# Performance work log

Measured on AMD Instinct MI355X. Metric: run time of the kernel, lower is better.

## Reference

```python
import jax, jax.numpy as jnp
import numpy as np

N_HEAD, D_MODEL, D_K, D_V = 8, 512, 64, 64
B, S = 4, 2048
LN_EPS = 1e-5


def setup_inputs() -> dict:
    key = jax.random.key(0)
    ks = jax.random.split(key, 12)
    std_qk = np.sqrt(2.0 / (D_MODEL + D_K))
    std_v = np.sqrt(2.0 / (D_MODEL + D_V))
    return {
        "q": jax.random.normal(ks[0], (B, S, D_MODEL), jnp.float32),
        "k": jax.random.normal(ks[1], (B, S, D_MODEL), jnp.float32),
        "v": jax.random.normal(ks[2], (B, S, D_MODEL), jnp.float32),
        "w_qs": jax.random.normal(ks[3], (N_HEAD * D_K, D_MODEL), jnp.float32) * std_qk,
        "b_qs": jnp.zeros((N_HEAD * D_K,), jnp.float32),
        "w_ks": jax.random.normal(ks[4], (N_HEAD * D_K, D_MODEL), jnp.float32) * std_qk,
        "b_ks": jnp.zeros((N_HEAD * D_K,), jnp.float32),
        "w_vs": jax.random.normal(ks[5], (N_HEAD * D_V, D_MODEL), jnp.float32) * std_v,
        "b_vs": jnp.zeros((N_HEAD * D_V,), jnp.float32),
        "w_fc": jax.random.normal(ks[6], (D_MODEL, N_HEAD * D_V), jnp.float32) * np.sqrt(2.0 / (D_MODEL + N_HEAD * D_V)),
        "b_fc": jnp.zeros((D_MODEL,), jnp.float32),
        "ln_g": jnp.ones((D_MODEL,), jnp.float32),
        "ln_b": jnp.zeros((D_MODEL,), jnp.float32),
    }


def reference(q, k, v, w_qs, b_qs, w_ks, b_ks, w_vs, b_vs, w_fc, b_fc, ln_g, ln_b):
    sz_b, len_q, _ = q.shape
    residual = q
    temperature = np.power(D_K, 0.5).astype(np.float32)
    # Projections: [b, s, h*dk] -> [h, b, s, dk]  (matches permute(2,0,1,3))
    qh = (jnp.einsum('bsd,fd->bsf', q, w_qs) + b_qs).reshape(sz_b, len_q, N_HEAD, D_K).transpose(2, 0, 1, 3)
    kh = (jnp.einsum('bsd,fd->bsf', k, w_ks) + b_ks).reshape(sz_b, -1, N_HEAD, D_K).transpose(2, 0, 1, 3)
    vh = (jnp.einsum('bsd,fd->bsf', v, w_vs) + b_vs).reshape(sz_b, -1, N_HEAD, D_V).transpose(2, 0, 1, 3)
    # Scaled dot-product attention (dropout is identity in eval)
    attn = jnp.einsum('hbqd,hbkd->hbqk', qh, kh) / temperature
    attn = jax.nn.softmax(attn, axis=-1)
    out = jnp.einsum('hbqk,hbkv->hbqv', attn, vh)          # [h, b, q, dv]
    out = out.transpose(1, 2, 0, 3).reshape(sz_b, len_q, N_HEAD * D_V)
    out = jnp.einsum('bsf,df->bsd', out, w_fc) + b_fc
    # Residual + LayerNorm
    x = out + residual
    mu = jnp.mean(x, axis=-1, keepdims=True)
    var = jnp.mean(jnp.square(x - mu), axis=-1, keepdims=True)
    x = (x - mu) * jax.lax.rsqrt(var + LN_EPS) * ln_g + ln_b
    # attn returned as [(n_head*b), len_q, len_k] to match torch bmm layout
    return x, attn.reshape(N_HEAD * sz_b, len_q, -1)
```

## Files before the change

kernel.cpp:

```cpp
#include <hip/hip_runtime.h>
#include <hip/hip_bf16.h>

constexpr int NB  = 4;
constexpr int NS  = 2048;
constexpr int NH  = 8;
constexpr int DM  = 512;
constexpr int DKV = 64;
constexpr int HB  = NH * NB;

typedef __attribute__((ext_vector_type(8))) short short8;
typedef __attribute__((ext_vector_type(4))) float f32x4;

__device__ inline unsigned short f2bf(float f) {
    unsigned u = __builtin_bit_cast(unsigned, f);
    u = (u + 0x7fffu + ((u >> 16) & 1u)) >> 16;
    return (unsigned short)u;
}
__device__ inline float bf2f(unsigned short h) {
    unsigned u = ((unsigned)h) << 16;
    return __builtin_bit_cast(float, u);
}
__device__ inline short8 ld8(const unsigned short* p) { return *(const short8*)p; }

__device__ inline short8 pack8(const float* p) {
    f32x4 a = *(const f32x4*)p;
    f32x4 b = *(const f32x4*)(p + 4);
    short8 r;
    r[0] = (short)f2bf(a[0]); r[1] = (short)f2bf(a[1]);
    r[2] = (short)f2bf(a[2]); r[3] = (short)f2bf(a[3]);
    r[4] = (short)f2bf(b[0]); r[5] = (short)f2bf(b[1]);
    r[6] = (short)f2bf(b[2]); r[7] = (short)f2bf(b[3]);
    return r;
}

__device__ inline f32x4 mfma16(short8 a, short8 b, f32x4 c) {
    return __builtin_amdgcn_mfma_f32_16x16x32_bf16(a, b, c, 0, 0, 0);
}

__device__ inline void gl_lds16(const void* g, void* l) {
    __builtin_amdgcn_global_load_lds(
        (const __attribute__((address_space(1))) unsigned*)g,
        (__attribute__((address_space(3))) unsigned*)l, 16, 0, 0);
}

__device__ inline void bar() { __builtin_amdgcn_s_barrier(); }

__global__ __launch_bounds__(256) void k_cvt(const float* __restrict__ x0,
                                             const float* __restrict__ x1,
                                             const float* __restrict__ x2,
                                             const float* __restrict__ w0,
                                             const float* __restrict__ w1,
                                             const float* __restrict__ w2,
                                             const float* __restrict__ w3,
                                             unsigned short* __restrict__ dx0,
                                             unsigned short* __restrict__ dx1,
                                             unsigned short* __restrict__ dx2,
                                             unsigned short* __restrict__ dw0,
                                             unsigned short* __restrict__ dw1,
                                             unsigned short* __restrict__ dw2,
                                             unsigned short* __restrict__ dw3)
{
    const float* s; unsigned short* d; size_t i;
    if (blockIdx.y < 3) {
        switch (blockIdx.y) {
            case 0:  s = x0; d = dx0; break;
            case 1:  s = x1; d = dx1; break;
            default: s = x2; d = dx2; break;
        }
        i = ((size_t)blockIdx.x * 256 + threadIdx.x) * 8;
    } else {
        if (blockIdx.x >= 512) return;
        switch (blockIdx.x >> 7) {
            case 0:  s = w0; d = dw0; break;
            case 1:  s = w1; d = dw1; break;
            case 2:  s = w2; d = dw2; break;
            default: s = w3; d = dw3; break;
        }
        i = ((size_t)(blockIdx.x & 127) * 256 + threadIdx.x) * 8;
    }
    *(short8*)(d + i) = pack8(s + i);
}

__global__ __launch_bounds__(256, 4) void k_proj(const unsigned short* __restrict__ X,
                                              const unsigned short* __restrict__ W,
                                              const float* __restrict__ bias,
                                              unsigned short* __restrict__ out,
                                              float scale, int vtrans)
{
    const int tid = threadIdx.x;
    const int l = tid & 63, w = tid >> 6;
    const int c = l & 15, g = l >> 4;
    const int m0 = blockIdx.y * 64 + w * 16;
    const int f0 = blockIdx.x * 64;
    const int arow = m0 + c;

    f32x4 acc[4] = {};
    const unsigned short* aB = X + (size_t)arow * DM;
    for (int kb = 0; kb < DM; kb += 32) {
        short8 af = ld8(aB + kb + g * 8);
#pragma unroll
        for (int n = 0; n < 4; ++n) {
            short8 bf = ld8(W + (size_t)(f0 + n * 16 + c) * DM + kb + g * 8);
            acc[n] = mfma16(af, bf, acc[n]);
        }
    }
#pragma unroll
    for (int n = 0; n < 4; ++n) {
        const int f = f0 + n * 16 + c;
        const int h = f >> 6, d = f & 63;
        const float bv = bias[f];
#pragma unroll
        for (int r = 0; r < 4; ++r) {
            const int m = m0 + g * 4 + r;
            const int bb = m >> 11, s = m & (NS - 1);
            const int hb = h * NB + bb;
            const float v = (acc[n][r] + bv) * scale;
            const size_t idx = vtrans ? ((size_t)(hb * DKV + d) * NS + s)
                                      : ((size_t)(hb * NS + s) * DKV + d);
            out[idx] = f2bf(v);
        }
    }
}

__global__ __launch_bounds__(256, 4) void k_attn(const unsigned short* __restrict__ Qh,
                                                 const unsigned short* __restrict__ Kh,
                                                 const unsigned short* __restrict__ Vt,
                                                 float* __restrict__ attn,
                                                 unsigned short* __restrict__ Obuf)
{
    __shared__ __align__(16) char kld[2][8192];
    __shared__ __align__(16) char vld[2][8192];
    __shared__ __align__(16) char plds[4 * 2048];
    const int tid = threadIdx.x;
    const int l = tid & 63, w = tid >> 6;
    const int c = l & 15, g = l >> 4;
    constexpr int NT = NS / 64;

    const int bid = blockIdx.x;
    const int wid = (bid & 7) * 128 + (bid >> 3);
    const int hb = wid >> 5;
    const int q0 = (wid & 31) * 64 + w * 16;
    char* myp = plds + w * 2048;

    const char* kbytes = (const char*)(Kh + (size_t)hb * NS * DKV);
    const char* vbytes = (const char*)(Vt + (size_t)hb * DKV * NS);

    const unsigned short* qb = Qh + ((size_t)hb * NS + q0 + c) * DKV + g * 8;
    const short8 qf0 = ld8(qb), qf1 = ld8(qb + 32);

    int koff[2], voff[2];
#pragma unroll
    for (int j = 0; j < 2; ++j) {
        const int D = (w * 2 + j) * 1024 + l * 16;
        const int row = D >> 7;
        const int scolb = (D & 127) ^ ((row & 7) << 4);
        koff[j] = row * 128 + scolb;
        voff[j] = row * (NS * 2) + scolb;
    }
    const int swc = (c & 7) << 4;

    const int ldsbase = w * 2048;

    float ls[4] = {0.f, 0.f, 0.f, 0.f};
    {
        gl_lds16(kbytes + koff[0], kld[0] + ldsbase);
        gl_lds16(kbytes + koff[1], kld[0] + ldsbase + 1024);
        asm volatile("s_waitcnt vmcnt(0)" ::: "memory");
        bar();
        __builtin_amdgcn_sched_barrier(0);
        int cur = 0;
        for (int kt = 0; kt < NT; ++kt) {
            if (kt + 1 < NT) {
                const size_t nb = (size_t)(kt + 1) * 64 * 128;
                gl_lds16(kbytes + nb + koff[0], kld[cur ^ 1] + ldsbase);
                gl_lds16(kbytes + nb + koff[1], kld[cur ^ 1] + ldsbase + 1024);
            }
            if (kt > 0) {
                if (kt + 1 < NT) { asm volatile("s_waitcnt vmcnt(2)" ::: "memory"); }
                else             { asm volatile("s_waitcnt vmcnt(0)" ::: "memory"); }
                bar();
                __builtin_amdgcn_sched_barrier(0);
            }
#pragma unroll
            for (int t = 0; t < 4; ++t) {
                const int rb = (t * 16 + c) * 128;
                const short8 b0 = *(const short8*)(kld[cur] + rb + ((g * 16) ^ swc));
                const short8 b1 = *(const short8*)(kld[cur] + rb + ((64 + g * 16) ^ swc));
                f32x4 z = {};
                z = mfma16(qf0, b0, z);
                z = mfma16(qf1, b1, z);
#pragma unroll
                for (int r = 0; r < 4; ++r) ls[r] += exp2f(z[r]);
            }
            bar();
            cur ^= 1;
        }
    }
    float li[4];
#pragma unroll
    for (int r = 0; r < 4; ++r) {
        float s = ls[r];
        s += __shfl_xor(s, 1);
        s += __shfl_xor(s, 2);
        s += __shfl_xor(s, 4);
        s += __shfl_xor(s, 8);
        li[r] = 1.0f / s;
    }

    f32x4 oacc[4] = {};
    const int srow = l >> 2, sseg = l & 3;
    float* srowp = attn + (size_t)hb * NS * NS + (size_t)(q0 + srow) * NS + sseg * 16;
    const int swsr = (srow & 7) << 4;

    {
        gl_lds16(kbytes + koff[0], kld[0] + ldsbase);
        gl_lds16(kbytes + koff[1], kld[0] + ldsbase + 1024);
        gl_lds16(vbytes + voff[0], vld[0] + ldsbase);
        gl_lds16(vbytes + voff[1], vld[0] + ldsbase + 1024);
        asm volatile("s_waitcnt vmcnt(0)" ::: "memory");
        bar();
        __builtin_amdgcn_sched_barrier(0);
        int cur = 0;
        for (int kt = 0; kt < NT; ++kt) {
            const int k0 = kt * 64;
            if (kt + 1 < NT) {
                const size_t nkb = (size_t)(k0 + 64) * 128;
                const size_t nvb = (size_t)(k0 + 64) * 2;
                gl_lds16(kbytes + nkb + koff[0], kld[cur ^ 1] + ldsbase);
                gl_lds16(kbytes + nkb + koff[1], kld[cur ^ 1] + ldsbase + 1024);
                gl_lds16(vbytes + nvb + voff[0], vld[cur ^ 1] + ldsbase);
                gl_lds16(vbytes + nvb + voff[1], vld[cur ^ 1] + ldsbase + 1024);
            }
            if (kt > 0) {
                if (kt + 1 < NT) { asm volatile("s_waitcnt vmcnt(8)" ::: "memory"); }
                else             { asm volatile("s_waitcnt vmcnt(4)" ::: "memory"); }
                bar();
                __builtin_amdgcn_sched_barrier(0);
            }
            f32x4 sc[4];
#pragma unroll
            for (int t = 0; t < 4; ++t) {
                const int rb = (t * 16 + c) * 128;
                const short8 b0 = *(const short8*)(kld[cur] + rb + ((g * 16) ^ swc));
                const short8 b1 = *(const short8*)(kld[cur] + rb + ((64 + g * 16) ^ swc));
                f32x4 z = {};
                z = mfma16(qf0, b0, z);
                z = mfma16(qf1, b1, z);
                sc[t] = z;
            }
#pragma unroll
            for (int t = 0; t < 4; ++t)
#pragma unroll
                for (int r = 0; r < 4; ++r) {
                    const float p = exp2f(sc[t][r]) * li[r];
                    const int row = g * 4 + r;
                    int by = row * 128 + (t * 16 + c) * 2;
                    by ^= (row & 7) << 4;
                    *(unsigned short*)(myp + by) = f2bf(p);
                }
            asm volatile("s_waitcnt lgkmcnt(0)" ::: "memory");
            __builtin_amdgcn_sched_barrier(0);
            {
                const short8 p0 = *(const short8*)(myp + srow * 128 + ((sseg * 32) ^ swsr));
                const short8 p1 = *(const short8*)(myp + srow * 128 + ((sseg * 32 + 16) ^ swsr));
                f32x4 o0, o1, o2, o3;
#pragma unroll
                for (int j = 0; j < 4; ++j) {
                    o0[j] = bf2f((unsigned short)p0[j]);
                    o1[j] = bf2f((unsigned short)p0[4 + j]);
                    o2[j] = bf2f((unsigned short)p1[j]);
                    o3[j] = bf2f((unsigned short)p1[4 + j]);
                }
                float* dst = srowp + k0;
                *(f32x4*)(dst)      = o0;
                *(f32x4*)(dst + 4)  = o1;
                *(f32x4*)(dst + 8)  = o2;
                *(f32x4*)(dst + 12) = o3;
            }
#pragma unroll
            for (int kk = 0; kk < 2; ++kk) {
                const short8 pa = *(const short8*)(myp + c * 128 + ((kk * 64 + g * 16) ^ swc));
#pragma unroll
                for (int n = 0; n < 4; ++n) {
                    const int rb = (n * 16 + c) * 128;
                    const short8 vb = *(const short8*)(vld[cur] + rb + ((kk * 64 + g * 16) ^ swc));
                    oacc[n] = mfma16(pa, vb, oacc[n]);
                }
            }
            bar();
            cur ^= 1;
        }
    }

    const int h = hb >> 2, bb = hb & 3;
#pragma unroll
    for (int n = 0; n < 4; ++n)
#pragma unroll
        for (int r = 0; r < 4; ++r) {
            const int q = q0 + g * 4 + r;
            const int dv = n * 16 + c;
            Obuf[((size_t)(bb * NS + q)) * DM + h * DKV + dv] = f2bf(oacc[n][r]);
        }
}

__global__ __launch_bounds__(256, 4) void k_fc(const unsigned short* __restrict__ O,
                                            const unsigned short* __restrict__ Wfc,
                                            const float* __restrict__ bfc,
                                            const float* __restrict__ resid,
                                            unsigned short* __restrict__ Y)
{
    const int tid = threadIdx.x;
    const int l = tid & 63, w = tid >> 6;
    const int c = l & 15, g = l >> 4;
    const int m0 = blockIdx.y * 64 + w * 16;
    const int f0 = blockIdx.x * 64;
    const int arow = m0 + c;

    f32x4 acc[4] = {};
    const unsigned short* aB = O + (size_t)arow * DM;
    for (int kb = 0; kb < DM; kb += 32) {
        short8 af = ld8(aB + kb + g * 8);
#pragma unroll
        for (int n = 0; n < 4; ++n) {
            short8 bf = ld8(Wfc + (size_t)(f0 + n * 16 + c) * DM + kb + g * 8);
            acc[n] = mfma16(af, bf, acc[n]);
        }
    }
#pragma unroll
    for (int n = 0; n < 4; ++n) {
        const int d = f0 + n * 16 + c;
        const float bv = bfc[d];
#pragma unroll
        for (int r = 0; r < 4; ++r) {
            const int m = m0 + g * 4 + r;
            const float v = acc[n][r] + bv + resid[(size_t)m * DM + d];
            Y[(size_t)m * DM + d] = f2bf(v);
        }
    }
}

__global__ __launch_bounds__(256) void k_ln(const unsigned short* __restrict__ Y,
                                            const float* __restrict__ gam,
                                            const float* __restrict__ bet,
                                            float* __restrict__ out)
{
    const int tid = threadIdx.x;
    const int l = tid & 63, w = tid >> 6;
    const int row = blockIdx.x * 4 + w;

    const short8 yv = ld8(Y + (size_t)row * DM + l * 8);
    float x[8];
#pragma unroll
    for (int j = 0; j < 8; ++j) x[j] = bf2f((unsigned short)yv[j]);

    float s = 0.f;
#pragma unroll
    for (int j = 0; j < 8; ++j) s += x[j];
#pragma unroll
    for (int mask = 1; mask <= 32; mask <<= 1) s += __shfl_xor(s, mask);
    const float mean = s * (1.0f / DM);

    float d2 = 0.f;
#pragma unroll
    for (int j = 0; j < 8; ++j) { const float t = x[j] - mean; d2 += t * t; }
#pragma unroll
    for (int mask = 1; mask <= 32; mask <<= 1) d2 += __shfl_xor(d2, mask);
    const float rstd = rsqrtf(d2 * (1.0f / DM) + 1e-5f);

#pragma unroll
    for (int j = 0; j < 8; ++j) {
        const int d = l * 8 + j;
        out[(size_t)row * DM + d] = (x[j] - mean) * rstd * gam[d] + bet[d];
    }
}

extern "C" void kernel_launch(void* const* d_in, const int* in_sizes, int n_in,
                              void* d_out, int out_size, void* d_ws, size_t ws_size,
                              hipStream_t stream)
{
    const float* q    = (const float*)d_in[0];
    const float* k    = (const float*)d_in[1];
    const float* v    = (const float*)d_in[2];
    const float* w_qs = (const float*)d_in[3];
    const float* b_qs = (const float*)d_in[4];
    const float* w_ks = (const float*)d_in[5];
    const float* b_ks = (const float*)d_in[6];
    const float* w_vs = (const float*)d_in[7];
    const float* b_vs = (const float*)d_in[8];
    const float* w_fc = (const float*)d_in[9];
    const float* b_fc = (const float*)d_in[10];
    const float* ln_g = (const float*)d_in[11];
    const float* ln_b = (const float*)d_in[12];

    char* ws = (char*)d_ws;
    unsigned short* Qh = (unsigned short*)(ws);
    unsigned short* Kh = (unsigned short*)(ws + (8u  << 20));
    unsigned short* Vt = (unsigned short*)(ws + (16u << 20));
    unsigned short* Ob = (unsigned short*)(ws + (24u << 20));
    unsigned short* Yb = (unsigned short*)(ws + (32u << 20));
    unsigned short* Wq = (unsigned short*)(ws + (40u << 20));
    unsigned short* Wk = Wq + (size_t)DM * DM;
    unsigned short* Wv = Wk + (size_t)DM * DM;
    unsigned short* Wf = Wv + (size_t)DM * DM;
    unsigned short* Xq = (unsigned short*)(ws + (48u << 20));
    unsigned short* Xk = (unsigned short*)(ws + (56u << 20));
    unsigned short* Xv = (unsigned short*)(ws + (64u << 20));

    float* xout = (float*)d_out;
    float* attn = xout + (size_t)NB * NS * DM;

    k_cvt<<<dim3(2048, 4), 256, 0, stream>>>(q, k, v, w_qs, w_ks, w_vs, w_fc,
                                             Xq, Xk, Xv, Wq, Wk, Wv, Wf);

    const float qscale = 0.125f * 1.44269504088896340736f;
    const dim3 gproj(8, 128);
    k_proj<<<gproj, 256, 0, stream>>>(Xq, Wq, b_qs, Qh, qscale, 0);
    k_proj<<<gproj, 256, 0, stream>>>(Xk, Wk, b_ks, Kh, 1.0f, 0);
    k_proj<<<gproj, 256, 0, stream>>>(Xv, Wv, b_vs, Vt, 1.0f, 1);

    k_attn<<<1024, 256, 0, stream>>>(Qh, Kh, Vt, attn, Ob);

    k_fc<<<gproj, 256, 0, stream>>>(Ob, Wf, b_fc, q, Yb);
    k_ln<<<NB * NS / 4, 256, 0, stream>>>(Yb, ln_g, ln_b, xout);
}
```

Baseline: 428.3 us.

## Fuse activation bf16 conversion into batched QKV projection and add MFMA priority hints

```diff
diff --git a/kernel.cpp b/kernel.cpp
--- a/kernel.cpp
+++ b/kernel.cpp
@@ -45,48 +45,47 @@
 
 __device__ inline void bar() { __builtin_amdgcn_s_barrier(); }
 
-__global__ __launch_bounds__(256) void k_cvt(const float* __restrict__ x0,
-                                             const float* __restrict__ x1,
-                                             const float* __restrict__ x2,
-                                             const float* __restrict__ w0,
-                                             const float* __restrict__ w1,
-                                             const float* __restrict__ w2,
-                                             const float* __restrict__ w3,
-                                             unsigned short* __restrict__ dx0,
-                                             unsigned short* __restrict__ dx1,
-                                             unsigned short* __restrict__ dx2,
-                                             unsigned short* __restrict__ dw0,
-                                             unsigned short* __restrict__ dw1,
-                                             unsigned short* __restrict__ dw2,
-                                             unsigned short* __restrict__ dw3)
-{
-    const float* s; unsigned short* d; size_t i;
-    if (blockIdx.y < 3) {
-        switch (blockIdx.y) {
-            case 0:  s = x0; d = dx0; break;
-            case 1:  s = x1; d = dx1; break;
-            default: s = x2; d = dx2; break;
-        }
-        i = ((size_t)blockIdx.x * 256 + threadIdx.x) * 8;
-    } else {
-        if (blockIdx.x >= 512) return;
-        switch (blockIdx.x >> 7) {
-            case 0:  s = w0; d = dw0; break;
-            case 1:  s = w1; d = dw1; break;
-            case 2:  s = w2; d = dw2; break;
-            default: s = w3; d = dw3; break;
-        }
-        i = ((size_t)(blockIdx.x & 127) * 256 + threadIdx.x) * 8;
-    }
+__global__ __launch_bounds__(256) void k_cvtw(const float* __restrict__ s0,
+                                              const float* __restrict__ s1,
+                                              const float* __restrict__ s2,
+                                              const float* __restrict__ s3,
+                                              unsigned short* __restrict__ d0,
+                                              unsigned short* __restrict__ d1,
+                                              unsigned short* __restrict__ d2,
+                                              unsigned short* __restrict__ d3)
+{
+    const float* s; unsigned short* d;
+    switch (blockIdx.y) {
+        case 0:  s = s0; d = d0; break;
+        case 1:  s = s1; d = d1; break;
+        case 2:  s = s2; d = d2; break;
+        default: s = s3; d = d3; break;
+    }
+    const size_t i = ((size_t)blockIdx.x * 256 + threadIdx.x) * 8;
     *(short8*)(d + i) = pack8(s + i);
 }
 
-__global__ __launch_bounds__(256, 4) void k_proj(const unsigned short* __restrict__ X,
-                                              const unsigned short* __restrict__ W,
-                                              const float* __restrict__ bias,
-                                              unsigned short* __restrict__ out,
-                                              float scale, int vtrans)
-{
+__global__ __launch_bounds__(256, 4) void k_proj3(const float* __restrict__ Xq,
+                                                  const float* __restrict__ Xk,
+                                                  const float* __restrict__ Xv,
+                                                  const unsigned short* __restrict__ Wq,
+                                                  const unsigned short* __restrict__ Wk,
+                                                  const unsigned short* __restrict__ Wv,
+                                                  const float* __restrict__ bq,
+                                                  const float* __restrict__ bk,
+                                                  const float* __restrict__ bv,
+                                                  unsigned short* __restrict__ oq,
+                                                  unsigned short* __restrict__ ok,
+                                                  unsigned short* __restrict__ ov)
+{
+    const float* X; const unsigned short* W; const float* bias; unsigned short* out;
+    float scale = 1.0f; int vtrans = 0;
+    switch (blockIdx.z) {
+        case 0:  X = Xq; W = Wq; bias = bq; out = oq;
+                 scale = 0.125f * 1.44269504088896340736f; break;
+        case 1:  X = Xk; W = Wk; bias = bk; out = ok; break;
+        default: X = Xv; W = Wv; bias = bv; out = ov; vtrans = 1; break;
+    }
     const int tid = threadIdx.x;
     const int l = tid & 63, w = tid >> 6;
     const int c = l & 15, g = l >> 4;
@@ -95,9 +94,9 @@
     const int arow = m0 + c;
 
     f32x4 acc[4] = {};
-    const unsigned short* aB = X + (size_t)arow * DM;
+    const float* aB = X + (size_t)arow * DM;
     for (int kb = 0; kb < DM; kb += 32) {
-        short8 af = ld8(aB + kb + g * 8);
+        short8 af = pack8(aB + kb + g * 8);
 #pragma unroll
         for (int n = 0; n < 4; ++n) {
             short8 bf = ld8(W + (size_t)(f0 + n * 16 + c) * DM + kb + g * 8);
@@ -108,13 +107,13 @@
     for (int n = 0; n < 4; ++n) {
         const int f = f0 + n * 16 + c;
         const int h = f >> 6, d = f & 63;
-        const float bv = bias[f];
+        const float bvv = bias[f];
 #pragma unroll
         for (int r = 0; r < 4; ++r) {
             const int m = m0 + g * 4 + r;
             const int bb = m >> 11, s = m & (NS - 1);
             const int hb = h * NB + bb;
-            const float v = (acc[n][r] + bv) * scale;
+            const float v = (acc[n][r] + bvv) * scale;
             const size_t idx = vtrans ? ((size_t)(hb * DKV + d) * NS + s)
                                       : ((size_t)(hb * NS + s) * DKV + d);
             out[idx] = f2bf(v);
@@ -181,6 +180,7 @@
                 bar();
                 __builtin_amdgcn_sched_barrier(0);
             }
+            __builtin_amdgcn_s_setprio(1);
 #pragma unroll
             for (int t = 0; t < 4; ++t) {
                 const int rb = (t * 16 + c) * 128;
@@ -192,6 +192,7 @@
 #pragma unroll
                 for (int r = 0; r < 4; ++r) ls[r] += exp2f(z[r]);
             }
+            __builtin_amdgcn_s_setprio(0);
             bar();
             cur ^= 1;
         }
@@ -238,6 +239,7 @@
                 __builtin_amdgcn_sched_barrier(0);
             }
             f32x4 sc[4];
+            __builtin_amdgcn_s_setprio(1);
 #pragma unroll
             for (int t = 0; t < 4; ++t) {
                 const int rb = (t * 16 + c) * 128;
@@ -248,6 +250,7 @@
                 z = mfma16(qf1, b1, z);
                 sc[t] = z;
             }
+            __builtin_amdgcn_s_setprio(0);
 #pragma unroll
             for (int t = 0; t < 4; ++t)
 #pragma unroll
@@ -277,6 +280,7 @@
                 *(f32x4*)(dst + 8)  = o2;
                 *(f32x4*)(dst + 12) = o3;
             }
+            __builtin_amdgcn_s_setprio(1);
 #pragma unroll
             for (int kk = 0; kk < 2; ++kk) {
                 const short8 pa = *(const short8*)(myp + c * 128 + ((kk * 64 + g * 16) ^ swc));
@@ -287,6 +291,7 @@
                     oacc[n] = mfma16(pa, vb, oacc[n]);
                 }
             }
+            __builtin_amdgcn_s_setprio(0);
             bar();
             cur ^= 1;
         }
@@ -402,24 +407,17 @@
     unsigned short* Wk = Wq + (size_t)DM * DM;
     unsigned short* Wv = Wk + (size_t)DM * DM;
     unsigned short* Wf = Wv + (size_t)DM * DM;
-    unsigned short* Xq = (unsigned short*)(ws + (48u << 20));
-    unsigned short* Xk = (unsigned short*)(ws + (56u << 20));
-    unsigned short* Xv = (unsigned short*)(ws + (64u << 20));
 
     float* xout = (float*)d_out;
     float* attn = xout + (size_t)NB * NS * DM;
 
-    k_cvt<<<dim3(2048, 4), 256, 0, stream>>>(q, k, v, w_qs, w_ks, w_vs, w_fc,
-                                             Xq, Xk, Xv, Wq, Wk, Wv, Wf);
-
-    const float qscale = 0.125f * 1.44269504088896340736f;
-    const dim3 gproj(8, 128);
-    k_proj<<<gproj, 256, 0, stream>>>(Xq, Wq, b_qs, Qh, qscale, 0);
-    k_proj<<<gproj, 256, 0, stream>>>(Xk, Wk, b_ks, Kh, 1.0f, 0);
-    k_proj<<<gproj, 256, 0, stream>>>(Xv, Wv, b_vs, Vt, 1.0f, 1);
+    k_cvtw<<<dim3(128, 4), 256, 0, stream>>>(w_qs, w_ks, w_vs, w_fc, Wq, Wk, Wv, Wf);
+
+    k_proj3<<<dim3(8, 128, 3), 256, 0, stream>>>(q, k, v, Wq, Wk, Wv,
+                                                 b_qs, b_ks, b_vs, Qh, Kh, Vt);
 
     k_attn<<<1024, 256, 0, stream>>>(Qh, Kh, Vt, attn, Ob);
 
-    k_fc<<<gproj, 256, 0, stream>>>(Ob, Wf, b_fc, q, Yb);
+    k_fc<<<dim3(8, 128), 256, 0, stream>>>(Ob, Wf, b_fc, q, Yb);
     k_ln<<<NB * NS / 4, 256, 0, stream>>>(Yb, ln_g, ln_b, xout);
 }
```

Measured after the change: 450.8 us. +5.3%, slower.
